# Kernel tuning notes

Hardware: AMD Instinct MI355X
Metric: run time of the kernel (lower is better)

Reference implementation:

```python
import jax, jax.numpy as jnp
import numpy as np

B, S, D = 4, 4096, 1024
EXPAND = 2
D_INNER = EXPAND * D          # 2048
D_CONV = 4
CHUNK = 64
H = 16
DH = D // H                   # 64
EPS = 1e-5


def setup_inputs() -> dict:
    key = jax.random.key(0)
    ks = jax.random.split(key, 10)
    s = 0.02
    return {
        "x": jax.random.normal(ks[0], (B, S, D), jnp.float32),
        "norm_w": jnp.ones((D,), jnp.float32),
        "w_up": jax.random.normal(ks[1], (D, D_INNER), jnp.float32) * s,
        "w_gate": jax.random.normal(ks[2], (D, D_INNER), jnp.float32) * s,
        "w_down": jax.random.normal(ks[3], (D_INNER, D), jnp.float32) * s,
        "conv_w": jax.random.normal(ks[4], (D_INNER, 1, D_CONV), jnp.float32) * s,
        "conv_b": jnp.zeros((D_INNER,), jnp.float32),
        "wq": jax.random.normal(ks[5], (D, D), jnp.float32) * s,
        "wk": jax.random.normal(ks[6], (D, D), jnp.float32) * s,
        "wv": jax.random.normal(ks[7], (D, D), jnp.float32) * s,
        "wo": jax.random.normal(ks[8], (D, D), jnp.float32) * s,
    }


def rmsnorm(x, w):
    var = jnp.mean(jnp.square(x.astype(jnp.float32)), axis=-1, keepdims=True)
    return (x * jax.lax.rsqrt(var + EPS).astype(x.dtype)) * w


def causal_dwconv(x, w, b):
    # x: [B, S, C] -> depthwise causal conv along S
    y = jax.lax.conv_general_dilated(
        x.transpose(0, 2, 1), w,
        window_strides=(1,), padding=[(D_CONV - 1, 0)],
        feature_group_count=D_INNER,
        dimension_numbers=("NCH", "OIH", "NCH"))
    return (y + b[None, :, None]).transpose(0, 2, 1)


def hebbian_memory(h, wq, wk, wv, wo):
    # chunked Hebbian associative memory: M += phi(k)^T v, read y = phi(q) M (+ intra-chunk causal)
    phi = lambda t: jax.nn.elu(t) + 1.0
    q = phi((h @ wq).reshape(B, S, H, DH)) * (DH ** -0.5)
    k = phi((h @ wk).reshape(B, S, H, DH))
    v = (h @ wv).reshape(B, S, H, DH)

    def to_chunks(t):  # [B,S,H,DH] -> [N, B, H, CHUNK, DH]
        return t.reshape(B, S // CHUNK, CHUNK, H, DH).transpose(1, 0, 3, 2, 4)

    qc, kc, vc = to_chunks(q), to_chunks(k), to_chunks(v)
    mask = jnp.tril(jnp.ones((CHUNK, CHUNK), bool))

    def step(M, inp):
        qb, kb, vb = inp                                   # [B,H,C,DH]
        inter = jnp.einsum("bhcd,bhde->bhce", qb, M)       # read from past memory
        sc = jnp.einsum("bhcd,bhed->bhce", qb, kb)
        sc = jnp.where(mask, sc, 0.0)                      # causal intra-chunk Hebbian read
        intra = jnp.einsum("bhce,bhed->bhcd", sc, vb)
        M = M + jnp.einsum("bhcd,bhce->bhde", kb, vb)      # Hebbian outer-product write
        return M, inter + intra

    M0 = jnp.zeros((B, H, DH, DH), h.dtype)
    _, y = jax.lax.scan(step, M0, (qc, kc, vc))            # y: [N,B,H,C,DH]
    y = y.transpose(1, 0, 3, 2, 4).reshape(B, S, D)
    return y @ wo


def reference(x, norm_w, w_up, w_gate, w_down, conv_w, conv_b, wq, wk, wv, wo):
    normed = rmsnorm(x, norm_w)
    val = jax.nn.silu(causal_dwconv(normed @ w_up, conv_w, conv_b))   # conv local mixing
    h = (jax.nn.silu(normed @ w_gate) * val) @ w_down                 # gated MLP
    out = hebbian_memory(h, wq, wk, wv, wo)                           # associative memory
    return x + out
```

## Files before the change

kernel.cpp:

```cpp
#include <hip/hip_runtime.h>
#include <hip/hip_fp16.h>
#include <cstdint>

#define NRALL 16384
#define DM    1024
#define DI    2048
#define SEQL  4096

typedef _Float16 f16;
typedef _Float16 f16x8 __attribute__((ext_vector_type(8)));
typedef _Float16 f16x4 __attribute__((ext_vector_type(4)));
typedef float    f32x4 __attribute__((ext_vector_type(4)));

__device__ __forceinline__ float phi_f(float t)  { return t > 0.0f ? t + 1.0f : __expf(t); }
__device__ __forceinline__ float silu_f(float t) { return t / (1.0f + __expf(-t)); }

#define GLDS16(g, l)                                                            \
    __builtin_amdgcn_global_load_lds(                                           \
        (const __attribute__((address_space(1))) void*)(g),                     \
        (__attribute__((address_space(3))) void*)(l), 16, 0, 0)

#define FMA4(dst, s, vv)                      \
    dst.x = fmaf((s), (vv).x, dst.x);         \
    dst.y = fmaf((s), (vv).y, dst.y);         \
    dst.z = fmaf((s), (vv).z, dst.z);         \
    dst.w = fmaf((s), (vv).w, dst.w);

__global__ __launch_bounds__(256) void rmsnorm_k(const float* __restrict__ x,
                                                 const float* __restrict__ nw,
                                                 f16* __restrict__ xn)
{
    const int r = blockIdx.x, t = threadIdx.x;
    const float4 v = *(const float4*)(x + (size_t)r * DM + t * 4);
    float s = v.x * v.x + v.y * v.y + v.z * v.z + v.w * v.w;
#pragma unroll
    for (int m = 1; m < 64; m <<= 1) s += __shfl_xor(s, m);
    __shared__ float ws4[4];
    if ((t & 63) == 0) ws4[t >> 6] = s;
    __syncthreads();
    const float tot = ws4[0] + ws4[1] + ws4[2] + ws4[3];
    const float sc = rsqrtf(tot * (1.0f / DM) + 1e-5f);
    const float4 w = *(const float4*)(nw + t * 4);
    f16x4 o;
    o[0] = (f16)(v.x * sc * w.x); o[1] = (f16)(v.y * sc * w.y);
    o[2] = (f16)(v.z * sc * w.z); o[3] = (f16)(v.w * sc * w.w);
    *(f16x4*)(xn + (size_t)r * DM + t * 4) = o;
}

__device__ __forceinline__ void wfmt_one(const float* __restrict__ W, char* __restrict__ fmt,
                                         int n, int kt, int Nw, int Ntot, int noff)
{
    const int ng = noff + n;
#pragma unroll
    for (int kh = 0; kh < 2; ++kh) {
        char* o = fmt + ((size_t)(kt * 2 + kh) * Ntot + ng) * 64;
#pragma unroll
        for (int c2 = 0; c2 < 4; ++c2) {
            f16x8 p;
#pragma unroll
            for (int j = 0; j < 8; ++j)
                p[j] = (f16)W[(size_t)(kt * 64 + kh * 32 + c2 * 8 + j) * Nw + n];
            *(f16x8*)(o + ((c2 ^ ((ng >> 1) & 3)) << 4)) = p;
        }
    }
}

__global__ __launch_bounds__(256) void wfmt_all_k(const float* __restrict__ w_up,
                                                  const float* __restrict__ w_gate,
                                                  const float* __restrict__ w_down,
                                                  const float* __restrict__ wq,
                                                  const float* __restrict__ wk,
                                                  const float* __restrict__ wv,
                                                  const float* __restrict__ wo,
                                                  char* __restrict__ fmtUG,
                                                  char* __restrict__ fmtD,
                                                  char* __restrict__ fmtQKV,
                                                  char* __restrict__ fmtO)
{
    int id = blockIdx.x;
    const int t = threadIdx.x;
    if (id < 128) { wfmt_one(w_up,   fmtUG,  (id % 8) * 256 + t, id / 8, DI, 4096, 0);    return; }
    id -= 128;
    if (id < 128) { wfmt_one(w_gate, fmtUG,  (id % 8) * 256 + t, id / 8, DI, 4096, 2048); return; }
    id -= 128;
    if (id < 128) { wfmt_one(w_down, fmtD,   (id % 4) * 256 + t, id / 4, DM, 1024, 0);    return; }
    id -= 128;
    if (id < 64)  { wfmt_one(wq,     fmtQKV, (id % 4) * 256 + t, id / 4, DM, 3072, 0);    return; }
    id -= 64;
    if (id < 64)  { wfmt_one(wk,     fmtQKV, (id % 4) * 256 + t, id / 4, DM, 3072, 1024); return; }
    id -= 64;
    if (id < 64)  { wfmt_one(wv,     fmtQKV, (id % 4) * 256 + t, id / 4, DM, 3072, 2048); return; }
    id -= 64;
    wfmt_one(wo, fmtO, (id % 4) * 256 + t, id / 4, DM, 1024, 0);
}

#define PREF_A(aset_, p, ks, rbase)                                               \
    _Pragma("unroll")                                                             \
    for (int q = 0; q < 4; ++q) {                                                 \
        const int row = wm * 128 + ((rbase) + q) * 16 + lr16;                     \
        afr[aset_][q] = *(const f16x8*)(ldsb + (p) * 32768 + (ks) * 16384         \
                        + row * 64 + ((kb ^ ((row >> 1) & 3)) << 4));             \
    }
#define PREF_B(bset_, p, ks)                                                      \
    _Pragma("unroll")                                                             \
    for (int q = 0; q < 4; ++q) {                                                 \
        const int n = wn * 64 + q * 16 + lr16;                                    \
        bfr[bset_][q] = *(const f16x8*)(ldsb + 65536 + (p) * 32768 + (ks) * 16384 \
                        + n * 64 + ((kb ^ ((n >> 1) & 3)) << 4));                 \
    }

#define PHASE(mh, AS, BS, PREF_STMT, STAGE_STMT, VM)                              \
    {                                                                             \
        asm volatile("s_waitcnt lgkmcnt(0)" ::: "memory");                        \
        __builtin_amdgcn_sched_barrier(0);                                        \
        if (VM) {                                                                 \
            asm volatile("s_waitcnt vmcnt(4)" ::: "memory");                      \
            __builtin_amdgcn_sched_barrier(0);                                    \
        }                                                                         \
        PREF_STMT;                                                                \
        STAGE_STMT;                                                               \
        __builtin_amdgcn_sched_barrier(0);                                        \
        __builtin_amdgcn_s_setprio(1);                                            \
        _Pragma("unroll")                                                         \
        for (int q = 0; q < 4; ++q) {                                             \
            acc[(mh) * 4 + q][0] = __builtin_amdgcn_mfma_f32_16x16x32_f16(        \
                afr[AS][q], bfr[BS][0], acc[(mh) * 4 + q][0], 0, 0, 0);           \
            acc[(mh) * 4 + q][1] = __builtin_amdgcn_mfma_f32_16x16x32_f16(        \
                afr[AS][q], bfr[BS][1], acc[(mh) * 4 + q][1], 0, 0, 0);           \
            acc[(mh) * 4 + q][2] = __builtin_amdgcn_mfma_f32_16x16x32_f16(        \
                afr[AS][q], bfr[BS][2], acc[(mh) * 4 + q][2], 0, 0, 0);           \
            acc[(mh) * 4 + q][3] = __builtin_amdgcn_mfma_f32_16x16x32_f16(        \
                afr[AS][q], bfr[BS][3], acc[(mh) * 4 + q][3], 0, 0, 0);           \
        }                                                                         \
        __builtin_amdgcn_s_setprio(0);                                            \
        __builtin_amdgcn_sched_barrier(0);                                        \
        __builtin_amdgcn_s_barrier();                                             \
    }

template <int EPI>
__global__ __launch_bounds__(512, 2) void mg256_k(const f16* __restrict__ A, int lda,
                                                  const char* __restrict__ fmt,
                                                  void* __restrict__ Cv,
                                                  int N, int K, int gx,
                                                  const float* __restrict__ addx)
{
    __shared__ __align__(16) char ldsb[131072];

    const int t = threadIdx.x;
    int wid = blockIdx.x;
    { const int cpx = gridDim.x >> 3; wid = (wid & 7) * cpx + (wid >> 3); }
    const int bx = wid % gx, by = wid / gx;
    const int bm = by * 256, bn = bx * 256;
    const int lane = t & 63, wv = t >> 6;
    const int wm = wv >> 2, wn = wv & 3;
    const int kb = lane >> 4, lr16 = lane & 15;
    const int NT = K >> 6;

    f32x4 acc[8][4];
#pragma unroll
    for (int i = 0; i < 8; ++i)
#pragma unroll
        for (int j = 0; j < 4; ++j) acc[i][j] = (f32x4)0.0f;

    auto STAGE_A = [&](int p, int kh, int kt) {
#pragma unroll
        for (int r = 0; r < 2; ++r) {
            const int idx = (r * 8 + wv) * 64;
            const int ii = idx + lane;
            const int row = ii >> 2, sl = ii & 3;
            const int c2 = sl ^ ((row >> 1) & 3);
            const f16* src = A + (size_t)(bm + row) * lda + kt * 64 + kh * 32 + c2 * 8;
            GLDS16(src, ldsb + p * 32768 + kh * 16384 + idx * 16);
        }
    };
    auto STAGE_B = [&](int p, int kh, int kt) {
#pragma unroll
        for (int r = 0; r < 2; ++r) {
            const int idx = (r * 8 + wv) * 64;
            const char* src = fmt + ((size_t)(kt * 2 + kh) * N + bn) * 64 + (size_t)(idx + lane) * 16;
            GLDS16(src, ldsb + 65536 + p * 32768 + kh * 16384 + idx * 16);
        }
    };

    f16x8 afr[2][4], bfr[2][4];

    const int T1 = NT > 1 ? 1 : 0;
    STAGE_B(0, 0, 0); STAGE_A(0, 0, 0); STAGE_B(0, 1, 0); STAGE_A(0, 1, 0);
    STAGE_B(1, 0, T1); STAGE_A(1, 0, T1); STAGE_B(1, 1, T1);
    asm volatile("s_waitcnt vmcnt(10)" ::: "memory");
    __builtin_amdgcn_s_barrier();
    __builtin_amdgcn_sched_barrier(0);
    PREF_A(0, 0, 0, 0);
    PREF_B(0, 0, 0);

    const int NI = NT >> 1;
    for (int i = 0; i < NI; ++i) {
        const int tc = 2 * i + 1;
        const int ta = 2 * i + 2 < NT ? 2 * i + 2 : NT - 1;
        const int tb = 2 * i + 3 < NT ? 2 * i + 3 : NT - 1;
        PHASE(0, 0, 0, PREF_A(1, 0, 0, 4),                    STAGE_A(1, 1, tc), 0)
        PHASE(1, 1, 0, PREF_A(0, 0, 1, 0); PREF_B(1, 0, 1),   STAGE_B(0, 0, ta), 1)
        PHASE(0, 0, 1, PREF_A(1, 0, 1, 4),                    STAGE_A(0, 0, ta), 0)
        PHASE(1, 1, 1, PREF_A(0, 1, 0, 0); PREF_B(0, 1, 0),   STAGE_B(0, 1, ta), 1)
        PHASE(0, 0, 0, PREF_A(1, 1, 0, 4),                    STAGE_A(0, 1, ta), 0)
        PHASE(1, 1, 0, PREF_A(0, 1, 1, 0); PREF_B(1, 1, 1),   STAGE_B(1, 0, tb), 1)
        PHASE(0, 0, 1, PREF_A(1, 1, 1, 4),                    STAGE_A(1, 0, tb), 0)
        PHASE(1, 1, 1, PREF_A(0, 0, 0, 0); PREF_B(0, 0, 0),   STAGE_B(1, 1, tb), 1)
    }
    asm volatile("s_waitcnt vmcnt(0)" ::: "memory");

#pragma unroll
    for (int fm = 0; fm < 8; ++fm) {
        const int row0 = bm + wm * 128 + fm * 16 + kb * 4;
#pragma unroll
        for (int fn = 0; fn < 4; ++fn) {
            const int col = bn + wn * 64 + fn * 16 + lr16;
#pragma unroll
            for (int r = 0; r < 4; ++r) {
                float o = acc[fm][fn][r];
                if (EPI == 1) {
                    if (col < DM) o = phi_f(o) * 0.125f;
                    else if (col < 2 * DM) o = phi_f(o);
                }
                if (EPI == 2) {
                    ((float*)Cv)[(size_t)(row0 + r) * N + col] =
                        o + addx[(size_t)(row0 + r) * N + col];
                } else {
                    ((f16*)Cv)[(size_t)(row0 + r) * N + col] = (f16)o;
                }
            }
        }
    }
}

__global__ __launch_bounds__(256) void conv_gate_k(f16* __restrict__ upg,
                                                   const float* __restrict__ cw,
                                                   const float* __restrict__ cb)
{
    const int r0 = blockIdx.x * 16;
    const int c = threadIdx.x * 8;
    float bias[8];
    {
        const float4 b0 = *(const float4*)(cb + c);
        const float4 b1 = *(const float4*)(cb + c + 4);
        bias[0] = b0.x; bias[1] = b0.y; bias[2] = b0.z; bias[3] = b0.w;
        bias[4] = b1.x; bias[5] = b1.y; bias[6] = b1.z; bias[7] = b1.w;
    }
    float tap[8][4];
#pragma unroll
    for (int j = 0; j < 8; ++j)
        *(float4*)tap[j] = *(const float4*)(cw + (size_t)(c + j) * 4);

    const bool lead = (r0 & (SEQL - 1)) == 0;
    f16x8 w0, w1, w2;
    if (lead) {
        w0 = (f16x8)(f16)0; w1 = (f16x8)(f16)0; w2 = (f16x8)(f16)0;
    } else {
        w0 = *(const f16x8*)(upg + (size_t)(r0 - 3) * 4096 + c);
        w1 = *(const f16x8*)(upg + (size_t)(r0 - 2) * 4096 + c);
        w2 = *(const f16x8*)(upg + (size_t)(r0 - 1) * 4096 + c);
    }
#pragma unroll 4
    for (int i = 0; i < 16; ++i) {
        const size_t row = (size_t)(r0 + i);
        const f16x8 w3 = *(const f16x8*)(upg + row * 4096 + c);
        const f16x8 g  = *(const f16x8*)(upg + row * 4096 + 2048 + c);
        f16x8 o;
#pragma unroll
        for (int j = 0; j < 8; ++j) {
            float a = bias[j];
            a = fmaf((float)w0[j], tap[j][0], a);
            a = fmaf((float)w1[j], tap[j][1], a);
            a = fmaf((float)w2[j], tap[j][2], a);
            a = fmaf((float)w3[j], tap[j][3], a);
            o[j] = (f16)(silu_f((float)g[j]) * silu_f(a));
        }
        *(f16x8*)(upg + row * 4096 + 2048 + c) = o;
        w0 = w1; w1 = w2; w2 = w3;
    }
}

__global__ __launch_bounds__(256) void gscan_g_k(const f16* __restrict__ qkv,
                                                 f16* __restrict__ G)
{
    __shared__ float Ks[4096];
    __shared__ float Vs[4096];
    const int t = threadIdx.x, ch = blockIdx.x, h = blockIdx.y, b = blockIdx.z;
    const int r = t >> 2, c16 = (t & 3) * 16;
    const f16* kp = qkv + ((size_t)b * SEQL + ch * 64 + r) * 3072 + DM + h * 64 + c16;
#pragma unroll
    for (int i = 0; i < 2; ++i) {
        const f16x8 kv = *(const f16x8*)(kp + 8 * i);
        const f16x8 vv = *(const f16x8*)(kp + DM + 8 * i);
#pragma unroll
        for (int j = 0; j < 8; ++j) {
            Ks[r * 64 + c16 + 8 * i + j] = (float)kv[j];
            Vs[r * 64 + c16 + 8 * i + j] = (float)vv[j];
        }
    }
    __syncthreads();
    const int d4 = (t >> 4) * 4, e4 = (t & 15) * 4;
    float4 ag[4] = {};
#pragma unroll 4
    for (int c = 0; c < 64; ++c) {
        float ka[4];
        *(float4*)ka = *(const float4*)(Ks + c * 64 + d4);
        const float4 va = *(const float4*)(Vs + c * 64 + e4);
        FMA4(ag[0], ka[0], va);
        FMA4(ag[1], ka[1], va);
        FMA4(ag[2], ka[2], va);
        FMA4(ag[3], ka[3], va);
    }
    f16* go = G + (((size_t)b * 16 + h) * 64 + ch) * 4096 + d4 * 64 + e4;
#pragma unroll
    for (int i = 0; i < 4; ++i) {
        f16x4 o;
        o[0] = (f16)ag[i].x; o[1] = (f16)ag[i].y;
        o[2] = (f16)ag[i].z; o[3] = (f16)ag[i].w;
        *(f16x4*)(go + i * 64) = o;
    }
}

__global__ __launch_bounds__(256) void gprefix_k(f16* __restrict__ G)
{
    const int bh = blockIdx.x >> 4, sl = blockIdx.x & 15;
    const int idx = sl * 256 + threadIdx.x;
    float run = 0.0f;
    f16* p = G + (size_t)bh * 64 * 4096 + idx;
#pragma unroll 4
    for (int ch = 0; ch < 64; ++ch) {
        const float g = (float)*p;
        *p = (f16)run;
        run += g;
        p += 4096;
    }
}

__global__ __launch_bounds__(256) void gscan_y_k(const f16* __restrict__ qkv,
                                                 const f16* __restrict__ G,
                                                 f16* __restrict__ y)
{
    __shared__ float qT[4096];
    __shared__ float Kd[4096];
    __shared__ float Vs[4096];
    __shared__ float Ms[4096];
    const int t = threadIdx.x, ch = blockIdx.x, h = blockIdx.y, b = blockIdx.z;
    const int r = t >> 2, c16 = (t & 3) * 16;
    const f16* qp = qkv + ((size_t)b * SEQL + ch * 64 + r) * 3072 + h * 64 + c16;
#pragma unroll
    for (int i = 0; i < 2; ++i) {
        const f16x8 qv = *(const f16x8*)(qp + 8 * i);
        const f16x8 kv = *(const f16x8*)(qp + DM + 8 * i);
        const f16x8 vv = *(const f16x8*)(qp + 2 * DM + 8 * i);
#pragma unroll
        for (int j = 0; j < 8; ++j) {
            qT[(c16 + 8 * i + j) * 64 + r] = (float)qv[j];
            Kd[(c16 + 8 * i + j) * 64 + r] = (float)kv[j];
            Vs[r * 64 + c16 + 8 * i + j] = (float)vv[j];
        }
    }
    const f16* mg = G + (((size_t)b * 16 + h) * 64 + ch) * 4096;
#pragma unroll
    for (int i = 0; i < 2; ++i) {
        const f16x8 mv = *(const f16x8*)(mg + t * 16 + 8 * i);
#pragma unroll
        for (int j = 0; j < 8; ++j) Ms[t * 16 + 8 * i + j] = (float)mv[j];
    }
    __syncthreads();

    const int c4 = (t >> 4) * 4, e4 = (t & 15) * 4;
    float sa[4][4] = {}, ya[4][4] = {};
#pragma unroll 2
    for (int d = 0; d < 64; ++d) {
        float a[4], bb[4], m[4];
        *(float4*)a = *(const float4*)(qT + d * 64 + c4);
        *(float4*)bb = *(const float4*)(Kd + d * 64 + e4);
        *(float4*)m = *(const float4*)(Ms + d * 64 + e4);
#pragma unroll
        for (int i = 0; i < 4; ++i)
#pragma unroll
            for (int j = 0; j < 4; ++j) {
                sa[i][j] = fmaf(a[i], bb[j], sa[i][j]);
                ya[i][j] = fmaf(a[i], m[j], ya[i][j]);
            }
    }
#pragma unroll
    for (int i = 0; i < 4; ++i)
#pragma unroll
        for (int j = 0; j < 4; ++j)
            if (e4 + j > c4 + i) sa[i][j] = 0.0f;
    __syncthreads();
#pragma unroll
    for (int i = 0; i < 4; ++i)
#pragma unroll
        for (int j = 0; j < 4; ++j)
            qT[(e4 + j) * 64 + c4 + i] = sa[i][j];
    __syncthreads();
#pragma unroll 2
    for (int e = 0; e < 64; ++e) {
        float a[4], vv[4];
        *(float4*)a = *(const float4*)(qT + e * 64 + c4);
        *(float4*)vv = *(const float4*)(Vs + e * 64 + e4);
#pragma unroll
        for (int i = 0; i < 4; ++i)
#pragma unroll
            for (int j = 0; j < 4; ++j)
                ya[i][j] = fmaf(a[i], vv[j], ya[i][j]);
    }
#pragma unroll
    for (int i = 0; i < 4; ++i) {
        f16x4 o;
        o[0] = (f16)ya[i][0]; o[1] = (f16)ya[i][1];
        o[2] = (f16)ya[i][2]; o[3] = (f16)ya[i][3];
        *(f16x4*)(y + ((size_t)b * SEQL + ch * 64 + c4 + i) * DM + h * 64 + e4) = o;
    }
}

extern "C" void kernel_launch(void* const* d_in, const int* in_sizes, int n_in,
                              void* d_out, int out_size, void* d_ws, size_t ws_size,
                              hipStream_t stream)
{
    const float* x      = (const float*)d_in[0];
    const float* norm_w = (const float*)d_in[1];
    const float* w_up   = (const float*)d_in[2];
    const float* w_gate = (const float*)d_in[3];
    const float* w_down = (const float*)d_in[4];
    const float* conv_w = (const float*)d_in[5];
    const float* conv_b = (const float*)d_in[6];
    const float* wq     = (const float*)d_in[7];
    const float* wk     = (const float*)d_in[8];
    const float* wv     = (const float*)d_in[9];
    const float* wo     = (const float*)d_in[10];
    float* out = (float*)d_out;

    const size_t BIG_NEED = 247463936ull;
    const bool big = ws_size >= BIG_NEED;

    if (big) {
        char* p = (char*)d_ws;
        f16* upg = (f16*)p;               p += (size_t)NRALL * 4096 * 2;
        f16* hb  = (f16*)p;               p += (size_t)NRALL * DM * 2;
        char* fmtD   = p;                 p += (size_t)64 * 1024 * 64;
        char* fmtQKV = p;                 p += (size_t)32 * 3072 * 64;
        char* fmtO   = p;                 p += (size_t)32 * 1024 * 64;
        f16* xn = (f16*)p;                p += (size_t)NRALL * DM * 2;
        char* fmtUG  = p;
        f16* G = (f16*)xn;
        f16* qkvb = upg;
        f16* yb   = hb;

        rmsnorm_k<<<NRALL, 256, 0, stream>>>(x, norm_w, xn);
        wfmt_all_k<<<640, 256, 0, stream>>>(w_up, w_gate, w_down, wq, wk, wv, wo,
                                            fmtUG, fmtD, fmtQKV, fmtO);

        mg256_k<0><<<16 * 64, 512, 0, stream>>>(xn, DM, fmtUG, upg, 4096, DM, 16, nullptr);
        conv_gate_k<<<NRALL / 16, 256, 0, stream>>>(upg, conv_w, conv_b);
        mg256_k<0><<<4 * 64, 512, 0, stream>>>(upg + 2048, 4096, fmtD, hb, 1024, DI, 4, nullptr);
        mg256_k<1><<<12 * 64, 512, 0, stream>>>(hb, DM, fmtQKV, qkvb, 3072, DM, 12, nullptr);

        gscan_g_k<<<dim3(64, 16, 4), 256, 0, stream>>>(qkvb, G);
        gprefix_k<<<1024, 256, 0, stream>>>(G);
        gscan_y_k<<<dim3(64, 16, 4), 256, 0, stream>>>(qkvb, G, yb);

        mg256_k<2><<<4 * 64, 512, 0, stream>>>(yb, DM, fmtO, out, 1024, DM, 4, x);
    } else {
        char* p = (char*)d_ws;
        f16* xn = (f16*)p;                p += (size_t)NRALL * DM * 2;
        f16* upg = (f16*)p;               p += (size_t)SEQL * 4096 * 2;
        f16* hb  = (f16*)p;               p += (size_t)SEQL * DM * 2;
        f16* G = (f16*)p;                 p += (size_t)16 * 64 * 4096 * 2;
        char* fmtUG  = p;                 p += (size_t)32 * 4096 * 64;
        char* fmtD   = p;                 p += (size_t)64 * 1024 * 64;
        char* fmtQKV = p;                 p += (size_t)32 * 3072 * 64;
        char* fmtO   = p;
        f16* qkvb = upg;
        f16* yb   = hb;

        rmsnorm_k<<<NRALL, 256, 0, stream>>>(x, norm_w, xn);
        wfmt_all_k<<<640, 256, 0, stream>>>(w_up, w_gate, w_down, wq, wk, wv, wo,
                                            fmtUG, fmtD, fmtQKV, fmtO);

        for (int b = 0; b < 4; ++b) {
            const f16* xnb = xn + (size_t)b * SEQL * DM;
            mg256_k<0><<<16 * 16, 512, 0, stream>>>(xnb, DM, fmtUG, upg, 4096, DM, 16, nullptr);
            conv_gate_k<<<SEQL / 16, 256, 0, stream>>>(upg, conv_w, conv_b);
            mg256_k<0><<<4 * 16, 512, 0, stream>>>(upg + 2048, 4096, fmtD, hb, 1024, DI, 4, nullptr);
            mg256_k<1><<<12 * 16, 512, 0, stream>>>(hb, DM, fmtQKV, qkvb, 3072, DM, 12, nullptr);
            gscan_g_k<<<dim3(64, 16, 1), 256, 0, stream>>>(qkvb, G);
            gprefix_k<<<256, 256, 0, stream>>>(G);
            gscan_y_k<<<dim3(64, 16, 1), 256, 0, stream>>>(qkvb, G, yb);
            mg256_k<2><<<4 * 16, 512, 0, stream>>>(yb, DM, fmtO,
                                                   out + (size_t)b * SEQL * DM, 1024, DM, 4,
                                                   x + (size_t)b * SEQL * DM);
        }
    }
}
```

Measured before the change: 612.9 us.

## Restructure GEMM main loop into four full-k-slice phases with simpler staging

```diff
diff --git a/kernel.cpp b/kernel.cpp
--- a/kernel.cpp
+++ b/kernel.cpp
@@ -94,43 +94,35 @@
     wfmt_one(wo, fmtO, (id % 4) * 256 + t, id / 4, DM, 1024, 0);
 }
 
-#define PREF_A(aset_, p, ks, rbase)                                               \
-    _Pragma("unroll")                                                             \
-    for (int q = 0; q < 4; ++q) {                                                 \
-        const int row = wm * 128 + ((rbase) + q) * 16 + lr16;                     \
-        afr[aset_][q] = *(const f16x8*)(ldsb + (p) * 32768 + (ks) * 16384         \
-                        + row * 64 + ((kb ^ ((row >> 1) & 3)) << 4));             \
-    }
-#define PREF_B(bset_, p, ks)                                                      \
-    _Pragma("unroll")                                                             \
-    for (int q = 0; q < 4; ++q) {                                                 \
-        const int n = wn * 64 + q * 16 + lr16;                                    \
-        bfr[bset_][q] = *(const f16x8*)(ldsb + 65536 + (p) * 32768 + (ks) * 16384 \
-                        + n * 64 + ((kb ^ ((n >> 1) & 3)) << 4));                 \
-    }
-
-#define PHASE(mh, AS, BS, PREF_STMT, STAGE_STMT, VM)                              \
+#define PH(p, ks, SP, SKH, ST)                                                    \
     {                                                                             \
+        asm volatile("s_waitcnt vmcnt(8)" ::: "memory");                          \
+        __builtin_amdgcn_sched_barrier(0);                                        \
+        _Pragma("unroll")                                                         \
+        for (int q = 0; q < 8; ++q) {                                             \
+            const int row = wm * 128 + q * 16 + lr16;                             \
+            af[q] = *(const f16x8*)(ldsb + (p) * 32768 + (ks) * 16384             \
+                    + row * 64 + ((kb ^ ((row >> 1) & 3)) << 4));                 \
+        }                                                                         \
+        _Pragma("unroll")                                                         \
+        for (int q = 0; q < 4; ++q) {                                             \
+            const int n = wn * 64 + q * 16 + lr16;                                \
+            bf[q] = *(const f16x8*)(ldsb + 65536 + (p) * 32768 + (ks) * 16384     \
+                    + n * 64 + ((kb ^ ((n >> 1) & 3)) << 4));                     \
+        }                                                                         \
+        STAGE_A(SP, SKH, ST);                                                     \
+        STAGE_B(SP, SKH, ST);                                                     \
+        __builtin_amdgcn_sched_barrier(0);                                        \
+        __builtin_amdgcn_s_barrier();                                             \
         asm volatile("s_waitcnt lgkmcnt(0)" ::: "memory");                        \
-        __builtin_amdgcn_sched_barrier(0);                                        \
-        if (VM) {                                                                 \
-            asm volatile("s_waitcnt vmcnt(4)" ::: "memory");                      \
-            __builtin_amdgcn_sched_barrier(0);                                    \
-        }                                                                         \
-        PREF_STMT;                                                                \
-        STAGE_STMT;                                                               \
         __builtin_amdgcn_sched_barrier(0);                                        \
         __builtin_amdgcn_s_setprio(1);                                            \
         _Pragma("unroll")                                                         \
-        for (int q = 0; q < 4; ++q) {                                             \
-            acc[(mh) * 4 + q][0] = __builtin_amdgcn_mfma_f32_16x16x32_f16(        \
-                afr[AS][q], bfr[BS][0], acc[(mh) * 4 + q][0], 0, 0, 0);           \
-            acc[(mh) * 4 + q][1] = __builtin_amdgcn_mfma_f32_16x16x32_f16(        \
-                afr[AS][q], bfr[BS][1], acc[(mh) * 4 + q][1], 0, 0, 0);           \
-            acc[(mh) * 4 + q][2] = __builtin_amdgcn_mfma_f32_16x16x32_f16(        \
-                afr[AS][q], bfr[BS][2], acc[(mh) * 4 + q][2], 0, 0, 0);           \
-            acc[(mh) * 4 + q][3] = __builtin_amdgcn_mfma_f32_16x16x32_f16(        \
-                afr[AS][q], bfr[BS][3], acc[(mh) * 4 + q][3], 0, 0, 0);           \
+        for (int q = 0; q < 8; ++q) {                                             \
+            acc[q][0] = __builtin_amdgcn_mfma_f32_16x16x32_f16(af[q], bf[0], acc[q][0], 0, 0, 0); \
+            acc[q][1] = __builtin_amdgcn_mfma_f32_16x16x32_f16(af[q], bf[1], acc[q][1], 0, 0, 0); \
+            acc[q][2] = __builtin_amdgcn_mfma_f32_16x16x32_f16(af[q], bf[2], acc[q][2], 0, 0, 0); \
+            acc[q][3] = __builtin_amdgcn_mfma_f32_16x16x32_f16(af[q], bf[3], acc[q][3], 0, 0, 0); \
         }                                                                         \
         __builtin_amdgcn_s_setprio(0);                                            \
         __builtin_amdgcn_sched_barrier(0);                                        \
@@ -182,30 +174,25 @@
         }
     };
 
-    f16x8 afr[2][4], bfr[2][4];
+    f16x8 af[8], bf[4];
 
     const int T1 = NT > 1 ? 1 : 0;
-    STAGE_B(0, 0, 0); STAGE_A(0, 0, 0); STAGE_B(0, 1, 0); STAGE_A(0, 1, 0);
-    STAGE_B(1, 0, T1); STAGE_A(1, 0, T1); STAGE_B(1, 1, T1);
-    asm volatile("s_waitcnt vmcnt(10)" ::: "memory");
+    STAGE_A(0, 0, 0); STAGE_B(0, 0, 0);
+    STAGE_A(0, 1, 0); STAGE_B(0, 1, 0);
+    STAGE_A(1, 0, T1); STAGE_B(1, 0, T1);
+    asm volatile("s_waitcnt vmcnt(8)" ::: "memory");
     __builtin_amdgcn_s_barrier();
     __builtin_amdgcn_sched_barrier(0);
-    PREF_A(0, 0, 0, 0);
-    PREF_B(0, 0, 0);
 
     const int NI = NT >> 1;
     for (int i = 0; i < NI; ++i) {
-        const int tc = 2 * i + 1;
-        const int ta = 2 * i + 2 < NT ? 2 * i + 2 : NT - 1;
-        const int tb = 2 * i + 3 < NT ? 2 * i + 3 : NT - 1;
-        PHASE(0, 0, 0, PREF_A(1, 0, 0, 4),                    STAGE_A(1, 1, tc), 0)
-        PHASE(1, 1, 0, PREF_A(0, 0, 1, 0); PREF_B(1, 0, 1),   STAGE_B(0, 0, ta), 1)
-        PHASE(0, 0, 1, PREF_A(1, 0, 1, 4),                    STAGE_A(0, 0, ta), 0)
-        PHASE(1, 1, 1, PREF_A(0, 1, 0, 0); PREF_B(0, 1, 0),   STAGE_B(0, 1, ta), 1)
-        PHASE(0, 0, 0, PREF_A(1, 1, 0, 4),                    STAGE_A(0, 1, ta), 0)
-        PHASE(1, 1, 0, PREF_A(0, 1, 1, 0); PREF_B(1, 1, 1),   STAGE_B(1, 0, tb), 1)
-        PHASE(0, 0, 1, PREF_A(1, 1, 1, 4),                    STAGE_A(1, 0, tb), 0)
-        PHASE(1, 1, 1, PREF_A(0, 0, 0, 0); PREF_B(0, 0, 0),   STAGE_B(1, 1, tb), 1)
+        const int tA = 2 * i + 1 < NT ? 2 * i + 1 : NT - 1;
+        const int tB = 2 * i + 2 < NT ? 2 * i + 2 : NT - 1;
+        const int tC = 2 * i + 3 < NT ? 2 * i + 3 : NT - 1;
+        PH(0, 0, 1, 1, tA)
+        PH(0, 1, 0, 0, tB)
+        PH(1, 0, 0, 1, tB)
+        PH(1, 1, 1, 0, tC)
     }
     asm volatile("s_waitcnt vmcnt(0)" ::: "memory");
 
```

Result: no change. 622.1 us (+1.5%).
